# Optimization experiments

Hardware: AMD Instinct MI355X
Metric: run time of the kernel (lower is better)

Reference implementation:

```python
import jax, jax.numpy as jnp
import numpy as np

N_USERS = 60000
N_ITEMS = 40000
N = N_USERS + N_ITEMS   # ncount
EMB = 64
NNZ = 3200000           # nnz of sparse_norm_adj (avg degree 32)
LN_EPS = 1e-5


def setup_inputs() -> dict:
    key = jax.random.key(0)
    ks = jax.random.split(key, 12)
    ego = jax.random.normal(ks[0], (N, EMB), jnp.float32) * 0.1
    rows = jax.random.randint(ks[1], (NNZ,), 0, N)
    cols = jax.random.randint(ks[2], (NNZ,), 0, N)
    # normalized adjacency values (non-trainable buffer)
    vals = jax.random.uniform(ks[3], (NNZ,), jnp.float32) * 0.01
    # xavier-uniform-ish scale for [64,64]: sqrt(2/(64+64)) = 0.125
    w_uu = jax.random.normal(ks[4], (EMB, EMB), jnp.float32) * 0.125
    filt_uu = jax.random.uniform(ks[5], (N_USERS,), jnp.float32, 0.99, 1.01)
    par_uu = jax.random.uniform(ks[6], (2,), jnp.float32, 0.0, 0.99)
    w_ii = jax.random.normal(ks[7], (EMB, EMB), jnp.float32) * 0.125
    filt_ii = jax.random.uniform(ks[8], (N_ITEMS,), jnp.float32, 0.99, 1.01)
    par_ii = jax.random.uniform(ks[9], (2,), jnp.float32, 0.0, 0.99)
    ln_gamma = jnp.ones((EMB,), jnp.float32)
    ln_beta = jnp.zeros((EMB,), jnp.float32)
    return {"ego_embeddings": ego, "rows": rows, "cols": cols, "vals": vals,
            "w_uu": w_uu, "filt_uu": filt_uu, "par_uu": par_uu,
            "w_ii": w_ii, "filt_ii": filt_ii, "par_ii": par_ii,
            "ln_gamma": ln_gamma, "ln_beta": ln_beta}


def _spmm(rows, cols, vals, x):
    # out[rows] += vals * x[cols]  <=>  sparse_adj @ x
    return jax.ops.segment_sum(vals[:, None] * x[cols], rows, num_segments=N)


def reference(ego_embeddings, rows, cols, vals, w_uu, filt_uu, par_uu,
              w_ii, filt_ii, par_ii, ln_gamma, ln_beta):
    res = ego_embeddings
    u = ego_embeddings[:N_USERS]
    it = ego_embeddings[N_USERS:]
    # HWNN layer with K1=K2=1 collapses to par0*par1 * diag(filter) @ X @ W
    user_ego = par_uu[0] * par_uu[1] * ((filt_uu[:, None] * u) @ w_uu) + u
    item_ego = par_ii[0] * par_ii[1] * ((filt_ii[:, None] * it) @ w_ii) + it
    ego = jnp.concatenate([user_ego, item_ego], axis=0)  # [N, EMB]
    # HGCNConv (act=False): adj @ (adj.T @ ego)
    h = jax.ops.segment_sum(vals[:, None] * ego[rows], cols, num_segments=N)  # adj.T @ ego
    y = _spmm(rows, cols, vals, h)                                            # adj @ h
    # LayerNorm (eps=1e-5, affine) + residual from the ORIGINAL input
    mu = jnp.mean(y, axis=-1, keepdims=True)
    var = jnp.var(y, axis=-1, keepdims=True)
    yn = (y - mu) / jnp.sqrt(var + LN_EPS) * ln_gamma + ln_beta
    out = yn + res
    return out[:N_USERS], out[N_USERS:]
```

## Files before the change

kernel.cpp:

```cpp
#include <hip/hip_runtime.h>

#define N_USERS 60000
#define N_ITEMS 40000
#define N_TOTAL 100000
#define EMB 64
#define LN_EPS 1e-5f

#define KPS 512
#define NSUP ((N_TOTAL + KPS - 1) / KPS)
#define EPB 4096
#define TR_ROWS 32
#define XPITCH 68

__device__ __forceinline__ float bf2f(unsigned short h)
{ return __uint_as_float(((unsigned)h) << 16); }
__device__ __forceinline__ unsigned short f2bf(float f)
{
    unsigned u = __float_as_uint(f);
    return (unsigned short)((u + 0x7FFFu + ((u >> 16) & 1u)) >> 16);
}

__global__ void transform_tile(const float* __restrict__ x,
                               const float* __restrict__ w_uu,
                               const float* __restrict__ filt_uu,
                               const float* __restrict__ par_uu,
                               const float* __restrict__ w_ii,
                               const float* __restrict__ filt_ii,
                               const float* __restrict__ par_ii,
                               unsigned short* __restrict__ out)
{
    __shared__ float Wls[EMB * EMB];
    __shared__ float xs[TR_ROWS * XPITCH];
    const int tid = threadIdx.x;
    const int r0 = blockIdx.x * TR_ROWS;
    const int itm = (r0 >= N_USERS);
    const float* W  = itm ? w_ii : w_uu;
    const float* fb = itm ? filt_ii : filt_uu;
    const int foff  = itm ? N_USERS : 0;
    const float c   = itm ? par_ii[0] * par_ii[1] : par_uu[0] * par_uu[1];

    for (int i = tid; i < EMB * EMB / 4; i += 256)
        ((float4*)Wls)[i] = ((const float4*)W)[i];
    for (int i = tid; i < TR_ROWS * 16; i += 256) {
        const float4 v = ((const float4*)x)[r0 * 16 + i];
        *(float4*)&xs[(i >> 4) * XPITCH + (i & 15) * 4] = v;
    }
    __syncthreads();

    const int lane = tid & 63;
    const int wv = tid >> 6;
    const int rg = lane >> 4;
    const int j  = lane & 15;

#pragma unroll
    for (int it = 0; it < 2; ++it) {
        const int rl = wv * 8 + it * 4 + rg;
        const int row = r0 + rl;
        float4 acc = make_float4(0.f, 0.f, 0.f, 0.f);
#pragma unroll 8
        for (int k = 0; k < EMB; ++k) {
            const float xb = xs[rl * XPITCH + k];
            const float4 w4 = *(const float4*)&Wls[k * EMB + 4 * j];
            acc.x += xb * w4.x; acc.y += xb * w4.y;
            acc.z += xb * w4.z; acc.w += xb * w4.w;
        }
        const float cf = c * fb[row - foff];
        const float4 xv = *(const float4*)&xs[rl * XPITCH + 4 * j];
        ushort4 o;
        o.x = f2bf(cf * acc.x + xv.x);
        o.y = f2bf(cf * acc.y + xv.y);
        o.z = f2bf(cf * acc.z + xv.z);
        o.w = f2bf(cf * acc.w + xv.w);
        *(ushort4*)&out[(size_t)row * EMB + 4 * j] = o;
    }
}

__global__ void hist_sup(const int* __restrict__ rows,
                         const int* __restrict__ cols,
                         int* __restrict__ cnt_r,
                         int* __restrict__ cnt_c, int nnz)
{
    __shared__ int hr[NSUP], hc[NSUP];
    const int tid = threadIdx.x;
    for (int i = tid; i < NSUP; i += 256) { hr[i] = 0; hc[i] = 0; }
    __syncthreads();
    for (int e = blockIdx.x * 256 + tid; e < nnz; e += gridDim.x * 256) {
        atomicAdd(&hr[rows[e] >> 9], 1);
        atomicAdd(&hc[cols[e] >> 9], 1);
    }
    __syncthreads();
    for (int i = tid; i < NSUP; i += 256) {
        if (hr[i]) atomicAdd(&cnt_r[i], hr[i]);
        if (hc[i]) atomicAdd(&cnt_c[i], hc[i]);
    }
}

__global__ void scan_sup(const int* __restrict__ cnt_c, int* __restrict__ base_c,
                         int* __restrict__ cur_c,
                         const int* __restrict__ cnt_r, int* __restrict__ base_r,
                         int* __restrict__ cur_r)
{
    const int* cnt = blockIdx.x ? cnt_r : cnt_c;
    int* base = blockIdx.x ? base_r : base_c;
    int* cur  = blockIdx.x ? cur_r  : cur_c;
    __shared__ int wsum[4];
    const int lane = threadIdx.x & 63;
    const int wv = threadIdx.x >> 6;
    const int i = threadIdx.x;
    const int v = (i < NSUP) ? cnt[i] : 0;
    int incl = v;
#pragma unroll
    for (int off = 1; off < 64; off <<= 1) {
        const int t = __shfl_up(incl, off, 64);
        if (lane >= off) incl += t;
    }
    if (lane == 63) wsum[wv] = incl;
    __syncthreads();
    int woff = 0;
    for (int w = 0; w < wv; ++w) woff += wsum[w];
    const int excl = woff + incl - v;
    if (i < NSUP) { base[i] = excl; cur[i] = excl; }
    if (i == 0) base[NSUP] = wsum[0] + wsum[1] + wsum[2] + wsum[3];
}

__global__ void __launch_bounds__(256, 1)
build_l1(const int* __restrict__ key,
         const int* __restrict__ other,
         const float* __restrict__ vals,
         int* __restrict__ cursor,
         int2* __restrict__ pairs1, int nnz)
{
    __shared__ int2 stage[EPB];
    __shared__ unsigned char sg[EPB];
    __shared__ int hist[NSUP];
    __shared__ int sexcl[NSUP];
    __shared__ int gbase[NSUP];
    __shared__ int lcur[NSUP];
    __shared__ int wsum[4];

    const int tid = threadIdx.x;
    const int e0 = blockIdx.x * EPB;
    const int ecnt = min(EPB, nnz - e0);

    for (int i = tid; i < NSUP; i += 256) hist[i] = 0;
    __syncthreads();

    int myk[16], myo[16];
    float myv[16];
#pragma unroll
    for (int i = 0; i < 16; ++i) {
        const int s = tid + i * 256;
        if (s < ecnt) {
            const int e = e0 + s;
            myk[i] = key[e]; myo[i] = other[e]; myv[i] = vals[e];
            atomicAdd(&hist[myk[i] >> 9], 1);
        } else myk[i] = -1;
    }
    __syncthreads();

    {
        const int lane = tid & 63;
        const int wv = tid >> 6;
        const int v = (tid < NSUP) ? hist[tid] : 0;
        int incl = v;
#pragma unroll
        for (int off = 1; off < 64; off <<= 1) {
            const int t = __shfl_up(incl, off, 64);
            if (lane >= off) incl += t;
        }
        if (lane == 63) wsum[wv] = incl;
        __syncthreads();
        int woff = 0;
        for (int w = 0; w < wv; ++w) woff += wsum[w];
        const int excl = woff + incl - v;
        if (tid < NSUP) {
            sexcl[tid] = excl;
            lcur[tid] = excl;
            gbase[tid] = v ? atomicAdd(&cursor[tid], v) : 0;
        }
    }
    __syncthreads();

#pragma unroll
    for (int i = 0; i < 16; ++i) {
        if (myk[i] >= 0) {
            const int g = myk[i] >> 9;
            const int s = atomicAdd(&lcur[g], 1);
            stage[s] = make_int2(myo[i] | ((myk[i] & (KPS - 1)) << 20),
                                 __float_as_int(myv[i]));
            sg[s] = (unsigned char)g;
        }
    }
    __syncthreads();

    for (int s = tid; s < ecnt; s += 256) {
        const int g = sg[s];
        pairs1[gbase[g] + (s - sexcl[g])] = stage[s];
    }
}

__global__ void sort_l2(const int* __restrict__ base,
                        const int2* __restrict__ pairs1,
                        int2* __restrict__ pairs2,
                        int* __restrict__ fine_ends)
{
    __shared__ int cnt[KPS];
    __shared__ int cur[KPS];
    __shared__ int csum[8];
    const int sup = blockIdx.x;
    const int beg = base[sup];
    const int end = base[sup + 1];
    const int tid = threadIdx.x;
    const int lane = tid & 63;
    const int wv = tid >> 6;

    if (tid < KPS) cnt[tid] = 0;
    __syncthreads();
    for (int j = beg + tid; j < end; j += 1024)
        atomicAdd(&cnt[pairs1[j].x >> 20], 1);
    __syncthreads();

    int orig = 0;
    if (wv < 8) {
        const int i = wv * 64 + lane;
        const int v = cnt[i];
        orig = v;
        int incl = v;
#pragma unroll
        for (int off = 1; off < 64; off <<= 1) {
            const int u = __shfl_up(incl, off, 64);
            if (lane >= off) incl += u;
        }
        cnt[i] = incl;
        if (lane == 63) csum[wv] = incl;
    }
    __syncthreads();
    if (tid == 0) {
        int run = 0;
#pragma unroll
        for (int c = 0; c < 8; ++c) { const int t = csum[c]; csum[c] = run; run += t; }
    }
    __syncthreads();
    if (wv < 8) {
        const int i = wv * 64 + lane;
        const int incl_g = csum[wv] + cnt[i];
        cur[i] = incl_g - orig;
        const int k = sup * KPS + i;
        if (k < N_TOTAL) fine_ends[k] = beg + incl_g;
    }
    __syncthreads();

    for (int j = beg + tid; j < end; j += 1024) {
        const int2 p = pairs1[j];
        const int pos = beg + atomicAdd(&cur[p.x >> 20], 1);
        pairs2[pos] = p;
    }
}

template <int U>
__device__ __forceinline__ void pull_step(const int2* __restrict__ pairs, int j,
                                          const unsigned short* __restrict__ src,
                                          int l, float4& acc)
{
    int2 p[U];
#pragma unroll
    for (int u = 0; u < U; ++u) p[u] = pairs[j + 4 * u];
    ushort4 s[U];
#pragma unroll
    for (int u = 0; u < U; ++u)
        s[u] = ((const ushort4*)(src + (size_t)(p[u].x & 0xFFFFF) * EMB))[l];
#pragma unroll
    for (int u = 0; u < U; ++u) {
        const float v = __int_as_float(p[u].y);
        acc.x += v * bf2f(s[u].x); acc.y += v * bf2f(s[u].y);
        acc.z += v * bf2f(s[u].z); acc.w += v * bf2f(s[u].w);
    }
}

__global__ void spmm_pull_bf16(const int* __restrict__ ends,
                               const int2* __restrict__ pairs,
                               const unsigned short* __restrict__ src,
                               unsigned short* __restrict__ dst, int nrows)
{
    const int lane = threadIdx.x & 63;
    const int wv = threadIdx.x >> 6;
    const int r = blockIdx.x * 4 + wv;
    if (r >= nrows) return;
    const int beg = (r == 0) ? 0 : ends[r - 1];
    const int end = ends[r];
    const int g = lane >> 4;
    const int l = lane & 15;
    float4 acc = make_float4(0.f, 0.f, 0.f, 0.f);
    int j = beg + g;
    for (; j + 28 < end; j += 32) pull_step<8>(pairs, j, src, l, acc);
    for (; j + 12 < end; j += 16) pull_step<4>(pairs, j, src, l, acc);
    for (; j < end; j += 4)       pull_step<1>(pairs, j, src, l, acc);
#pragma unroll
    for (int m = 16; m <= 32; m <<= 1) {
        acc.x += __shfl_xor(acc.x, m, 64);
        acc.y += __shfl_xor(acc.y, m, 64);
        acc.z += __shfl_xor(acc.z, m, 64);
        acc.w += __shfl_xor(acc.w, m, 64);
    }
    if (g == 0) {
        ushort4 o;
        o.x = f2bf(acc.x); o.y = f2bf(acc.y);
        o.z = f2bf(acc.z); o.w = f2bf(acc.w);
        ((ushort4*)(dst + (size_t)r * EMB))[l] = o;
    }
}

__global__ void spmm_pull_ln(const int* __restrict__ ends,
                             const int2* __restrict__ pairs,
                             const unsigned short* __restrict__ src,
                             const float* __restrict__ ego,
                             const float* __restrict__ gamma,
                             const float* __restrict__ beta,
                             float* __restrict__ out, int nrows)
{
    const int lane = threadIdx.x & 63;
    const int wv = threadIdx.x >> 6;
    const int r = blockIdx.x * 4 + wv;
    if (r >= nrows) return;
    const int beg = (r == 0) ? 0 : ends[r - 1];
    const int end = ends[r];
    const int g = lane >> 4;
    const int l = lane & 15;
    float4 acc = make_float4(0.f, 0.f, 0.f, 0.f);
    int j = beg + g;
    for (; j + 28 < end; j += 32) pull_step<8>(pairs, j, src, l, acc);
    for (; j + 12 < end; j += 16) pull_step<4>(pairs, j, src, l, acc);
    for (; j < end; j += 4)       pull_step<1>(pairs, j, src, l, acc);
#pragma unroll
    for (int m = 16; m <= 32; m <<= 1) {
        acc.x += __shfl_xor(acc.x, m, 64);
        acc.y += __shfl_xor(acc.y, m, 64);
        acc.z += __shfl_xor(acc.z, m, 64);
        acc.w += __shfl_xor(acc.w, m, 64);
    }
    float s  = acc.x + acc.y + acc.z + acc.w;
    float s2 = acc.x * acc.x + acc.y * acc.y + acc.z * acc.z + acc.w * acc.w;
#pragma unroll
    for (int m = 1; m <= 8; m <<= 1) {
        s  += __shfl_xor(s,  m, 64);
        s2 += __shfl_xor(s2, m, 64);
    }
    const float mu  = s * (1.0f / EMB);
    const float var = s2 * (1.0f / EMB) - mu * mu;
    const float inv = rsqrtf(var + LN_EPS);
    if (g == 0) {
        const float4 gm = ((const float4*)gamma)[l];
        const float4 bt = ((const float4*)beta)[l];
        const float4 eg = ((const float4*)(ego + (size_t)r * EMB))[l];
        float4 o;
        o.x = (acc.x - mu) * inv * gm.x + bt.x + eg.x;
        o.y = (acc.y - mu) * inv * gm.y + bt.y + eg.y;
        o.z = (acc.z - mu) * inv * gm.z + bt.z + eg.z;
        o.w = (acc.w - mu) * inv * gm.w + bt.w + eg.w;
        ((float4*)(out + (size_t)r * EMB))[l] = o;
    }
}

__global__ void transform_kernel(const float* __restrict__ x,
                                 const float* __restrict__ W,
                                 const float* __restrict__ filt,
                                 const float* __restrict__ par,
                                 float* __restrict__ out, int nrows)
{
    __shared__ float Ws[EMB * EMB];
    const int tid = threadIdx.x;
    for (int i = tid; i < EMB * EMB; i += blockDim.x) Ws[i] = W[i];
    __syncthreads();
    const float c = par[0] * par[1];
    const int lane = tid & 63;
    const int wave = tid >> 6;
    const int r0 = blockIdx.x * 32;
    for (int rr = wave; rr < 32; rr += 4) {
        const int r = r0 + rr;
        if (r >= nrows) break;
        const float xv = x[(size_t)r * EMB + lane];
        float acc = 0.f;
#pragma unroll
        for (int k = 0; k < EMB; ++k) {
            const float xk = __shfl(xv, k, 64);
            acc += xk * Ws[k * EMB + lane];
        }
        out[(size_t)r * EMB + lane] = c * filt[r] * acc + xv;
    }
}

__global__ void spmm_scatter(const int* __restrict__ src_idx,
                             const int* __restrict__ dst_idx,
                             const float* __restrict__ vals,
                             const float* __restrict__ src,
                             float* __restrict__ dst, int nnz)
{
    const long long t = (long long)blockIdx.x * blockDim.x + threadIdx.x;
    const int e = (int)(t >> 4);
    const int l = (int)(t & 15);
    if (e >= nnz) return;
    const int s = src_idx[e];
    const int d = dst_idx[e];
    const float v = vals[e];
    const float4 xv = ((const float4*)(src + (size_t)s * EMB))[l];
    float* dp = dst + (size_t)d * EMB + l * 4;
    atomicAdd(dp + 0, v * xv.x);
    atomicAdd(dp + 1, v * xv.y);
    atomicAdd(dp + 2, v * xv.z);
    atomicAdd(dp + 3, v * xv.w);
}

__global__ void ln_residual(const float* y,
                            const float* __restrict__ ego,
                            const float* __restrict__ gamma,
                            const float* __restrict__ beta,
                            float* out, int nrows)
{
    const int lane = threadIdx.x & 63;
    const int wave = threadIdx.x >> 6;
    const int r = blockIdx.x * 4 + wave;
    if (r >= nrows) return;
    const float v = y[(size_t)r * EMB + lane];
    float s = v, s2 = v * v;
#pragma unroll
    for (int off = 32; off > 0; off >>= 1) {
        s  += __shfl_down(s,  off, 64);
        s2 += __shfl_down(s2, off, 64);
    }
    s  = __shfl(s,  0, 64);
    s2 = __shfl(s2, 0, 64);
    const float mu  = s * (1.0f / EMB);
    const float var = s2 * (1.0f / EMB) - mu * mu;
    const float inv = rsqrtf(var + LN_EPS);
    out[(size_t)r * EMB + lane] =
        (v - mu) * inv * gamma[lane] + beta[lane] + ego[(size_t)r * EMB + lane];
}

extern "C" void kernel_launch(void* const* d_in, const int* in_sizes, int n_in,
                              void* d_out, int out_size, void* d_ws, size_t ws_size,
                              hipStream_t stream)
{
    const float* ego     = (const float*)d_in[0];
    const int*   rows    = (const int*)  d_in[1];
    const int*   cols    = (const int*)  d_in[2];
    const float* vals    = (const float*)d_in[3];
    const float* w_uu    = (const float*)d_in[4];
    const float* filt_uu = (const float*)d_in[5];
    const float* par_uu  = (const float*)d_in[6];
    const float* w_ii    = (const float*)d_in[7];
    const float* filt_ii = (const float*)d_in[8];
    const float* par_ii  = (const float*)d_in[9];
    const float* gamma   = (const float*)d_in[10];
    const float* beta    = (const float*)d_in[11];
    float* out = (float*)d_out;
    const int nnz = in_sizes[1];

    const size_t emb_elems = (size_t)N_TOTAL * EMB;
    const size_t emb_bytes = emb_elems * sizeof(float);

    const size_t need = 2 * emb_bytes + (size_t)nnz * sizeof(int2)
                        + 2 * (size_t)N_TOTAL * sizeof(int);

    const int rb = (N_TOTAL + 3) / 4;

    if (ws_size >= need) {
        unsigned short* ego2b = (unsigned short*)d_ws;
        unsigned short* hb    = ego2b + emb_elems;
        int2*  pairs1    = (int2*)(hb + emb_elems);
        int2*  pairs2    = pairs1 + nnz;
        int*   fine_ends = (int*)(pairs2 + nnz);
        int*   cnt_c  = fine_ends + N_TOTAL;
        int*   cnt_r  = cnt_c + NSUP;
        int*   base_c = cnt_r + NSUP;
        int*   cur_c  = base_c + (NSUP + 1);
        int*   base_r = cur_c + NSUP;
        int*   cur_r  = base_r + (NSUP + 1);

        hipMemsetAsync(cnt_c, 0, 2 * NSUP * sizeof(int), stream);

        hist_sup<<<512, 256, 0, stream>>>(rows, cols, cnt_r, cnt_c, nnz);
        scan_sup<<<2, 256, 0, stream>>>(cnt_c, base_c, cur_c,
                                        cnt_r, base_r, cur_r);

        transform_tile<<<N_TOTAL / TR_ROWS, 256, 0, stream>>>(
            ego, w_uu, filt_uu, par_uu, w_ii, filt_ii, par_ii, ego2b);

        const int l1b = (nnz + EPB - 1) / EPB;

        build_l1<<<l1b, 256, 0, stream>>>(cols, rows, vals, cur_c, pairs1, nnz);
        sort_l2<<<NSUP, 1024, 0, stream>>>(base_c, pairs1, pairs2, fine_ends);
        spmm_pull_bf16<<<rb, 256, 0, stream>>>(fine_ends, pairs2, ego2b, hb,
                                               N_TOTAL);

        build_l1<<<l1b, 256, 0, stream>>>(rows, cols, vals, cur_r, pairs1, nnz);
        sort_l2<<<NSUP, 1024, 0, stream>>>(base_r, pairs1, pairs2, fine_ends);
        spmm_pull_ln<<<rb, 256, 0, stream>>>(fine_ends, pairs2, hb,
                                             ego, gamma, beta, out, N_TOTAL);
    } else {
        float* ego2 = (float*)d_ws;
        float* h    = ego2 + emb_elems;
        hipMemsetAsync(h,   0, emb_bytes, stream);
        hipMemsetAsync(out, 0, emb_bytes, stream);

        transform_kernel<<<(N_USERS + 31) / 32, 256, 0, stream>>>(
            ego, w_uu, filt_uu, par_uu, ego2, N_USERS);
        transform_kernel<<<(N_ITEMS + 31) / 32, 256, 0, stream>>>(
            ego + (size_t)N_USERS * EMB, w_ii, filt_ii, par_ii,
            ego2 + (size_t)N_USERS * EMB, N_ITEMS);

        const long long thr = (long long)nnz * 16;
        const int sblocks = (int)((thr + 255) / 256);
        spmm_scatter<<<sblocks, 256, 0, stream>>>(rows, cols, vals, ego2, h, nnz);
        spmm_scatter<<<sblocks, 256, 0, stream>>>(cols, rows, vals, h, out, nnz);

        ln_residual<<<rb, 256, 0, stream>>>(out, ego, gamma, beta, out, N_TOTAL);
    }
}
```

Before: 432.7 us.

## Widen SpMM gathers to 16-byte loads and drop LDS staging in bucket scatter

The two pull-SpMM kernels now have each lane load a uint4 (8 bf16 values) instead of a ushort4, so 8 edges are processed in parallel per wave with 8 lanes per row, and accumulation uses two float4s. The LayerNorm reduction and epilogue are adjusted to match. build_l1 drops the shared-memory staging buffer and local prefix scan and writes pairs directly to global memory at atomically assigned offsets. This cuts shared memory use and removes the extra pass, but the direct global writes are less coalesced. Entries within a bucket are also no longer ordered deterministically.

Result: no change. 436.3 us (+0.8%).

```diff
diff --git a/kernel.cpp b/kernel.cpp
--- a/kernel.cpp
+++ b/kernel.cpp
@@ -19,6 +19,10 @@
     unsigned u = __float_as_uint(f);
     return (unsigned short)((u + 0x7FFFu + ((u >> 16) & 1u)) >> 16);
 }
+__device__ __forceinline__ float blo(unsigned w)
+{ return __uint_as_float(w << 16); }
+__device__ __forceinline__ float bhi(unsigned w)
+{ return __uint_as_float(w & 0xFFFF0000u); }
 
 __global__ void transform_tile(const float* __restrict__ x,
                                const float* __restrict__ w_uu,
@@ -123,20 +127,15 @@
     if (i == 0) base[NSUP] = wsum[0] + wsum[1] + wsum[2] + wsum[3];
 }
 
-__global__ void __launch_bounds__(256, 1)
-build_l1(const int* __restrict__ key,
-         const int* __restrict__ other,
-         const float* __restrict__ vals,
-         int* __restrict__ cursor,
-         int2* __restrict__ pairs1, int nnz)
-{
-    __shared__ int2 stage[EPB];
-    __shared__ unsigned char sg[EPB];
+__global__ void build_l1(const int* __restrict__ key,
+                         const int* __restrict__ other,
+                         const float* __restrict__ vals,
+                         int* __restrict__ cursor,
+                         int2* __restrict__ pairs1, int nnz)
+{
     __shared__ int hist[NSUP];
-    __shared__ int sexcl[NSUP];
     __shared__ int gbase[NSUP];
     __shared__ int lcur[NSUP];
-    __shared__ int wsum[4];
 
     const int tid = threadIdx.x;
     const int e0 = blockIdx.x * EPB;
@@ -158,26 +157,10 @@
     }
     __syncthreads();
 
-    {
-        const int lane = tid & 63;
-        const int wv = tid >> 6;
-        const int v = (tid < NSUP) ? hist[tid] : 0;
-        int incl = v;
-#pragma unroll
-        for (int off = 1; off < 64; off <<= 1) {
-            const int t = __shfl_up(incl, off, 64);
-            if (lane >= off) incl += t;
-        }
-        if (lane == 63) wsum[wv] = incl;
-        __syncthreads();
-        int woff = 0;
-        for (int w = 0; w < wv; ++w) woff += wsum[w];
-        const int excl = woff + incl - v;
-        if (tid < NSUP) {
-            sexcl[tid] = excl;
-            lcur[tid] = excl;
-            gbase[tid] = v ? atomicAdd(&cursor[tid], v) : 0;
-        }
+    for (int i = tid; i < NSUP; i += 256) {
+        const int v = hist[i];
+        gbase[i] = v ? atomicAdd(&cursor[i], v) : 0;
+        lcur[i] = 0;
     }
     __syncthreads();
 
@@ -185,17 +168,11 @@
     for (int i = 0; i < 16; ++i) {
         if (myk[i] >= 0) {
             const int g = myk[i] >> 9;
-            const int s = atomicAdd(&lcur[g], 1);
-            stage[s] = make_int2(myo[i] | ((myk[i] & (KPS - 1)) << 20),
-                                 __float_as_int(myv[i]));
-            sg[s] = (unsigned char)g;
+            const int o = atomicAdd(&lcur[g], 1);
+            pairs1[gbase[g] + o] =
+                make_int2(myo[i] | ((myk[i] & (KPS - 1)) << 20),
+                          __float_as_int(myv[i]));
         }
-    }
-    __syncthreads();
-
-    for (int s = tid; s < ecnt; s += 256) {
-        const int g = sg[s];
-        pairs1[gbase[g] + (s - sexcl[g])] = stage[s];
     }
 }
 
@@ -258,22 +235,24 @@
 }
 
 template <int U>
-__device__ __forceinline__ void pull_step(const int2* __restrict__ pairs, int j,
-                                          const unsigned short* __restrict__ src,
-                                          int l, float4& acc)
+__device__ __forceinline__ void pull_step8(const int2* __restrict__ pairs, int j,
+                                           const unsigned short* __restrict__ src,
+                                           int l, float4& a0, float4& a1)
 {
     int2 p[U];
 #pragma unroll
-    for (int u = 0; u < U; ++u) p[u] = pairs[j + 4 * u];
-    ushort4 s[U];
+    for (int u = 0; u < U; ++u) p[u] = pairs[j + 8 * u];
+    uint4 s[U];
 #pragma unroll
     for (int u = 0; u < U; ++u)
-        s[u] = ((const ushort4*)(src + (size_t)(p[u].x & 0xFFFFF) * EMB))[l];
+        s[u] = ((const uint4*)(src + (size_t)(p[u].x & 0xFFFFF) * EMB))[l];
 #pragma unroll
     for (int u = 0; u < U; ++u) {
         const float v = __int_as_float(p[u].y);
-        acc.x += v * bf2f(s[u].x); acc.y += v * bf2f(s[u].y);
-        acc.z += v * bf2f(s[u].z); acc.w += v * bf2f(s[u].w);
+        a0.x += v * blo(s[u].x); a0.y += v * bhi(s[u].x);
+        a0.z += v * blo(s[u].y); a0.w += v * bhi(s[u].y);
+        a1.x += v * blo(s[u].z); a1.y += v * bhi(s[u].z);
+        a1.z += v * blo(s[u].w); a1.w += v * bhi(s[u].w);
     }
 }
 
@@ -288,25 +267,27 @@
     if (r >= nrows) return;
     const int beg = (r == 0) ? 0 : ends[r - 1];
     const int end = ends[r];
-    const int g = lane >> 4;
-    const int l = lane & 15;
-    float4 acc = make_float4(0.f, 0.f, 0.f, 0.f);
+    const int g = lane >> 3;
+    const int l = lane & 7;
+    float4 a0 = make_float4(0.f, 0.f, 0.f, 0.f);
+    float4 a1 = make_float4(0.f, 0.f, 0.f, 0.f);
     int j = beg + g;
-    for (; j + 28 < end; j += 32) pull_step<8>(pairs, j, src, l, acc);
-    for (; j + 12 < end; j += 16) pull_step<4>(pairs, j, src, l, acc);
-    for (; j < end; j += 4)       pull_step<1>(pairs, j, src, l, acc);
-#pragma unroll
-    for (int m = 16; m <= 32; m <<= 1) {
-        acc.x += __shfl_xor(acc.x, m, 64);
-        acc.y += __shfl_xor(acc.y, m, 64);
-        acc.z += __shfl_xor(acc.z, m, 64);
-        acc.w += __shfl_xor(acc.w, m, 64);
+    for (; j + 24 < end; j += 32) pull_step8<4>(pairs, j, src, l, a0, a1);
+    for (; j < end; j += 8)       pull_step8<1>(pairs, j, src, l, a0, a1);
+#pragma unroll
+    for (int m = 8; m <= 32; m <<= 1) {
+        a0.x += __shfl_xor(a0.x, m, 64); a0.y += __shfl_xor(a0.y, m, 64);
+        a0.z += __shfl_xor(a0.z, m, 64); a0.w += __shfl_xor(a0.w, m, 64);
+        a1.x += __shfl_xor(a1.x, m, 64); a1.y += __shfl_xor(a1.y, m, 64);
+        a1.z += __shfl_xor(a1.z, m, 64); a1.w += __shfl_xor(a1.w, m, 64);
     }
     if (g == 0) {
-        ushort4 o;
-        o.x = f2bf(acc.x); o.y = f2bf(acc.y);
-        o.z = f2bf(acc.z); o.w = f2bf(acc.w);
-        ((ushort4*)(dst + (size_t)r * EMB))[l] = o;
+        uint4 o;
+        o.x = (unsigned)f2bf(a0.x) | ((unsigned)f2bf(a0.y) << 16);
+        o.y = (unsigned)f2bf(a0.z) | ((unsigned)f2bf(a0.w) << 16);
+        o.z = (unsigned)f2bf(a1.x) | ((unsigned)f2bf(a1.y) << 16);
+        o.w = (unsigned)f2bf(a1.z) | ((unsigned)f2bf(a1.w) << 16);
+        ((uint4*)(dst + (size_t)r * EMB))[l] = o;
     }
 }
 
@@ -324,24 +305,25 @@
     if (r >= nrows) return;
     const int beg = (r == 0) ? 0 : ends[r - 1];
     const int end = ends[r];
-    const int g = lane >> 4;
-    const int l = lane & 15;
-    float4 acc = make_float4(0.f, 0.f, 0.f, 0.f);
+    const int g = lane >> 3;
+    const int l = lane & 7;
+    float4 a0 = make_float4(0.f, 0.f, 0.f, 0.f);
+    float4 a1 = make_float4(0.f, 0.f, 0.f, 0.f);
     int j = beg + g;
-    for (; j + 28 < end; j += 32) pull_step<8>(pairs, j, src, l, acc);
-    for (; j + 12 < end; j += 16) pull_step<4>(pairs, j, src, l, acc);
-    for (; j < end; j += 4)       pull_step<1>(pairs, j, src, l, acc);
-#pragma unroll
-    for (int m = 16; m <= 32; m <<= 1) {
-        acc.x += __shfl_xor(acc.x, m, 64);
-        acc.y += __shfl_xor(acc.y, m, 64);
-        acc.z += __shfl_xor(acc.z, m, 64);
-        acc.w += __shfl_xor(acc.w, m, 64);
-    }
-    float s  = acc.x + acc.y + acc.z + acc.w;
-    float s2 = acc.x * acc.x + acc.y * acc.y + acc.z * acc.z + acc.w * acc.w;
-#pragma unroll
-    for (int m = 1; m <= 8; m <<= 1) {
+    for (; j + 24 < end; j += 32) pull_step8<4>(pairs, j, src, l, a0, a1);
+    for (; j < end; j += 8)       pull_step8<1>(pairs, j, src, l, a0, a1);
+#pragma unroll
+    for (int m = 8; m <= 32; m <<= 1) {
+        a0.x += __shfl_xor(a0.x, m, 64); a0.y += __shfl_xor(a0.y, m, 64);
+        a0.z += __shfl_xor(a0.z, m, 64); a0.w += __shfl_xor(a0.w, m, 64);
+        a1.x += __shfl_xor(a1.x, m, 64); a1.y += __shfl_xor(a1.y, m, 64);
+        a1.z += __shfl_xor(a1.z, m, 64); a1.w += __shfl_xor(a1.w, m, 64);
+    }
+    float s  = a0.x + a0.y + a0.z + a0.w + a1.x + a1.y + a1.z + a1.w;
+    float s2 = a0.x * a0.x + a0.y * a0.y + a0.z * a0.z + a0.w * a0.w
+             + a1.x * a1.x + a1.y * a1.y + a1.z * a1.z + a1.w * a1.w;
+#pragma unroll
+    for (int m = 1; m <= 4; m <<= 1) {
         s  += __shfl_xor(s,  m, 64);
         s2 += __shfl_xor(s2, m, 64);
     }
@@ -349,15 +331,23 @@
     const float var = s2 * (1.0f / EMB) - mu * mu;
     const float inv = rsqrtf(var + LN_EPS);
     if (g == 0) {
-        const float4 gm = ((const float4*)gamma)[l];
-        const float4 bt = ((const float4*)beta)[l];
-        const float4 eg = ((const float4*)(ego + (size_t)r * EMB))[l];
-        float4 o;
-        o.x = (acc.x - mu) * inv * gm.x + bt.x + eg.x;
-        o.y = (acc.y - mu) * inv * gm.y + bt.y + eg.y;
-        o.z = (acc.z - mu) * inv * gm.z + bt.z + eg.z;
-        o.w = (acc.w - mu) * inv * gm.w + bt.w + eg.w;
-        ((float4*)(out + (size_t)r * EMB))[l] = o;
+        const float4 gmA = ((const float4*)gamma)[2 * l];
+        const float4 gmB = ((const float4*)gamma)[2 * l + 1];
+        const float4 btA = ((const float4*)beta)[2 * l];
+        const float4 btB = ((const float4*)beta)[2 * l + 1];
+        const float4 egA = ((const float4*)(ego + (size_t)r * EMB))[2 * l];
+        const float4 egB = ((const float4*)(ego + (size_t)r * EMB))[2 * l + 1];
+        float4 oA, oB;
+        oA.x = (a0.x - mu) * inv * gmA.x + btA.x + egA.x;
+        oA.y = (a0.y - mu) * inv * gmA.y + btA.y + egA.y;
+        oA.z = (a0.z - mu) * inv * gmA.z + btA.z + egA.z;
+        oA.w = (a0.w - mu) * inv * gmA.w + btA.w + egA.w;
+        oB.x = (a1.x - mu) * inv * gmB.x + btB.x + egB.x;
+        oB.y = (a1.y - mu) * inv * gmB.y + btB.y + egB.y;
+        oB.z = (a1.z - mu) * inv * gmB.z + btB.z + egB.z;
+        oB.w = (a1.w - mu) * inv * gmB.w + btB.w + egB.w;
+        ((float4*)(out + (size_t)r * EMB))[2 * l]     = oA;
+        ((float4*)(out + (size_t)r * EMB))[2 * l + 1] = oB;
     }
 }
 
```
